# Performance work log

Measured on AMD Instinct MI355X. Metric: run time of the kernel, lower is better.

The kernel has to match this reference:

```python
import jax, jax.numpy as jnp
import numpy as np

F_DIM = 64; HID = 64; HEADS = 2; DH = 32; NG = 4; EPS = 1e-5; SCALE = 8.0  # sqrt(hid_dim)
B = 4; H = 64; W = 64; S = 8; CIN = 64


def _ln(x, g, b):
    mu = x.mean(-1, keepdims=True)
    var = ((x - mu) ** 2).mean(-1, keepdims=True)
    return (x - mu) * jax.lax.rsqrt(var + EPS) * g + b


def _gn(x, g, b):
    # x: [b, C, H, W]; normalize per group over (C/NG, H, W)
    bb, c, hh, ww = x.shape
    xg = x.reshape(bb, NG, -1)
    mu = xg.mean(-1, keepdims=True)
    var = ((xg - mu) ** 2).mean(-1, keepdims=True)
    xn = ((xg - mu) * jax.lax.rsqrt(var + EPS)).reshape(bb, c, hh, ww)
    return xn * g[None, :, None, None] + b[None, :, None, None]


def _mha(xq, xkv, qw, qb, kw, kb, vw, vb, ow, ob):
    # per-head attention with scaling by sqrt(hid_dim) (as in the source)
    q = xq @ qw + qb
    k = xkv @ kw + kb
    v = xkv @ vw + vb
    bb, l, _ = q.shape
    m = k.shape[1]
    qh = q.reshape(bb, l, HEADS, DH)
    kh = k.reshape(bb, m, HEADS, DH)
    vh = v.reshape(bb, m, HEADS, DH)
    s = jnp.einsum('blhd,bmhd->bhlm', qh, kh) / SCALE
    p = jax.nn.softmax(s, axis=-1)
    z = jnp.einsum('bhlm,bmhd->blhd', p, vh).reshape(bb, l, HID)
    return z @ ow + ob


def setup_inputs() -> dict:
    key = jax.random.key(0)
    ks = jax.random.split(key, 34)
    p = lambda k, shp: (jax.random.normal(k, shp, jnp.float32) * 0.02)
    d = {
        'x': jax.random.normal(ks[0], (B, H, W, F_DIM), jnp.float32),
        'slots': jax.random.normal(ks[1], (B, S, CIN), jnp.float32),
        'conv1_w': p(ks[2], (F_DIM, F_DIM)), 'conv1_b': p(ks[3], (F_DIM,)),
        'conv2_w': p(ks[4], (F_DIM, F_DIM)), 'conv2_b': p(ks[5], (F_DIM,)),
        'gn_g': jnp.ones((F_DIM,), jnp.float32), 'gn_b': jnp.zeros((F_DIM,), jnp.float32),
        'ln2_g': jnp.ones((F_DIM,), jnp.float32), 'ln2_b': jnp.zeros((F_DIM,), jnp.float32),
        'ln3_g': jnp.ones((F_DIM,), jnp.float32), 'ln3_b': jnp.zeros((F_DIM,), jnp.float32),
        'ln4_g': jnp.ones((F_DIM,), jnp.float32), 'ln4_b': jnp.zeros((F_DIM,), jnp.float32),
        'sa_qw': p(ks[6], (F_DIM, HID)), 'sa_qb': p(ks[7], (HID,)),
        'sa_kw': p(ks[8], (F_DIM, HID)), 'sa_kb': p(ks[9], (HID,)),
        'sa_vw': p(ks[10], (F_DIM, HID)), 'sa_vb': p(ks[11], (HID,)),
        'sa_ow': p(ks[12], (HID, F_DIM)), 'sa_ob': p(ks[13], (F_DIM,)),
        'ca_qw': p(ks[14], (F_DIM, HID)), 'ca_qb': p(ks[15], (HID,)),
        'ca_kw': p(ks[16], (CIN, HID)), 'ca_kb': p(ks[17], (HID,)),
        'ca_vw': p(ks[18], (CIN, HID)), 'ca_vb': p(ks[19], (HID,)),
        'ca_ow': p(ks[20], (HID, F_DIM)), 'ca_ob': p(ks[21], (F_DIM,)),
        'ff1_w': p(ks[22], (F_DIM, F_DIM)), 'ff1_b': p(ks[23], (F_DIM,)),
    }
    return d


def reference(x, slots, conv1_w, conv1_b, conv2_w, conv2_b, gn_g, gn_b,
              ln2_g, ln2_b, ln3_g, ln3_b, ln4_g, ln4_b,
              sa_qw, sa_qb, sa_kw, sa_kb, sa_vw, sa_vb, sa_ow, sa_ob,
              ca_qw, ca_qb, ca_kw, ca_kb, ca_vw, ca_vb, ca_ow, ca_ob,
              ff1_w, ff1_b):
    b, h, w, f = x.shape
    xc = jnp.transpose(x, (0, 3, 1, 2))               # [b,f,h,w]
    xc = _gn(xc, gn_g, gn_b)
    xc = jnp.einsum('bchw,oc->bohw', xc, conv1_w) + conv1_b[None, :, None, None]
    # faithful to torch: .contiguous().view(b,-1,f) on channels-first layout
    xs = xc.reshape(b, h * w, f)
    # repeat = 1
    xs = jax.nn.gelu(_ln(_mha(xs, xs, sa_qw, sa_qb, sa_kw, sa_kb, sa_vw, sa_vb, sa_ow, sa_ob), ln2_g, ln2_b) + xs, approximate=False)
    xs = _ln(_mha(xs, slots, ca_qw, ca_qb, ca_kw, ca_kb, ca_vw, ca_vb, ca_ow, ca_ob), ln3_g, ln3_b) + xs
    xs = _ln(xs @ ff1_w + ff1_b, ln4_g, ln4_b) + xs
    xo = jnp.transpose(xs.reshape(b, h, w, f), (0, 3, 1, 2))
    xo = jnp.einsum('bchw,oc->bohw', xo, conv2_w) + conv2_b[None, :, None, None]
    return jnp.transpose(xo, (0, 2, 3, 1))
```

## Files before the change

### kernel.cpp

```cpp
#include <hip/hip_runtime.h>
#include <hip/hip_bf16.h>
#include <math.h>

#define NBATCH 4
#define LTOK   4096
#define FD     64
#define NIT    16

typedef __attribute__((ext_vector_type(8))) short short8v;
typedef __attribute__((ext_vector_type(4))) float f32x4;

static __device__ inline uint32_t packbf2(float a, float b) {
    float2 f; f.x = a; f.y = b;
    __hip_bfloat162 h = __float22bfloat162_rn(f);
    uint32_t u; __builtin_memcpy(&u, &h, 4);
    return u;
}
static __device__ inline ushort packbf1(float a) {
    __hip_bfloat16 h = __float2bfloat16(a);
    ushort u; __builtin_memcpy(&u, &h, 2);
    return u;
}
static __device__ inline float gelu_exact(float y) {
    return 0.5f * y * (1.0f + erff(y * 0.70710678118654752f));
}

__global__ void gn_part_kernel(const float* __restrict__ x,
                               float* __restrict__ partS, float* __restrict__ partSS) {
    const int b = blockIdx.x >> 6, c = blockIdx.x & 63;
    const int t = threadIdx.x, l = t & 63, wv = t >> 6;
    const float4* xb = (const float4*)(x + (size_t)b * 262144) + (size_t)c * 1024;
    float s = 0.f, ss = 0.f;
#pragma unroll
    for (int k = 0; k < 4; k++) {
        float4 v = xb[t + 256 * k];
        s += (v.x + v.y) + (v.z + v.w);
        ss += (v.x * v.x + v.y * v.y) + (v.z * v.z + v.w * v.w);
    }
#pragma unroll
    for (int o = 0; o < 4; o++) {
        const int off = (int[]){1, 2, 16, 32}[o];
        s += __shfl_xor(s, off, 64);
        ss += __shfl_xor(ss, off, 64);
    }
    __shared__ float ls_s[4][4], ls_ss[4][4];
    if ((l & 51) == 0) { ls_s[wv][(l >> 2) & 3] = s; ls_ss[wv][(l >> 2) & 3] = ss; }
    __syncthreads();
    if (t < 4) {
        float S = 0.f, SS = 0.f;
#pragma unroll
        for (int w2 = 0; w2 < 4; w2++) { S += ls_s[w2][t]; SS += ls_ss[w2][t]; }
        partS[b * 256 + t * 64 + c] = S;
        partSS[b * 256 + t * 64 + c] = SS;
    }
}

__global__ void gn_conv1_kernel(const float* __restrict__ x,
                                const float* __restrict__ partS, const float* __restrict__ partSS,
                                const float* __restrict__ gg, const float* __restrict__ gb,
                                const float* __restrict__ w, const float* __restrict__ bias,
                                float* __restrict__ out) {
    const int b = blockIdx.x >> 6, i = blockIdx.x & 63;
    const int t = threadIdx.x;
    __shared__ float xn[64][65];
    __shared__ float wsm[64][64];
    __shared__ float sm[4], sr[4];
    {
        float sv = partS[b * 256 + t];
        float ssv = partSS[b * 256 + t];
        for (int o = 32; o; o >>= 1) { sv += __shfl_xor(sv, o, 64); ssv += __shfl_xor(ssv, o, 64); }
        if ((t & 63) == 0) {
            float mean = sv * (1.f / 65536.f);
            float var = ssv * (1.f / 65536.f) - mean * mean;
            sm[t >> 6] = mean;
            sr[t >> 6] = rsqrtf(var + 1e-5f);
        }
    }
    __syncthreads();
    {
        const int j = t >> 2, c0 = (t & 3) * 16, g = c0 >> 4;
        const float mean = sm[g], rstd = sr[g];
        const float* src = x + (((size_t)b * 64 + i) * 64 + j) * 64 + c0;
#pragma unroll
        for (int k = 0; k < 4; k++) {
            float4 v = *(const float4*)(src + 4 * k);
            xn[j][c0 + 4 * k + 0] = (v.x - mean) * rstd * gg[c0 + 4 * k + 0] + gb[c0 + 4 * k + 0];
            xn[j][c0 + 4 * k + 1] = (v.y - mean) * rstd * gg[c0 + 4 * k + 1] + gb[c0 + 4 * k + 1];
            xn[j][c0 + 4 * k + 2] = (v.z - mean) * rstd * gg[c0 + 4 * k + 2] + gb[c0 + 4 * k + 2];
            xn[j][c0 + 4 * k + 3] = (v.w - mean) * rstd * gg[c0 + 4 * k + 3] + gb[c0 + 4 * k + 3];
        }
        const int o = t >> 2, cc0 = (t & 3) * 16;
#pragma unroll
        for (int k = 0; k < 16; k++) wsm[cc0 + k][o] = w[o * 64 + cc0 + k];
    }
    __syncthreads();
    const int jj = t & 63, olo = (t >> 6) * 16;
    float acc[16];
#pragma unroll
    for (int oi = 0; oi < 16; oi++) acc[oi] = bias[olo + oi];
    for (int c = 0; c < 64; c++) {
        float xv = xn[jj][c];
#pragma unroll
        for (int oi = 0; oi < 16; oi++) acc[oi] += xv * wsm[c][olo + oi];
    }
#pragma unroll
    for (int oi = 0; oi < 16; oi++)
        out[((size_t)b * LTOK + (size_t)(olo + oi) * 64 + i) * 64 + jj] = acc[oi];
}

__global__ void qkv_kernel(const float* __restrict__ in,
                           const float* __restrict__ qw, const float* __restrict__ qb,
                           const float* __restrict__ kw, const float* __restrict__ kb,
                           const float* __restrict__ vw, const float* __restrict__ vb,
                           ushort* __restrict__ Qo, ushort* __restrict__ Ko, ushort* __restrict__ VTg) {
    __shared__ float xt[64][68];
    __shared__ float wt[64][64];
    __shared__ ushort vtr[64 * 72];
    const int t = threadIdx.x;
    const int ph = blockIdx.y;
    const size_t tok0 = (size_t)blockIdx.x * 64;
    const int b = blockIdx.x >> 6;
    const int tokb0 = (blockIdx.x & 63) * 64;
    const int r = t >> 2, cq = t & 3, olo = cq * 16;
    const float* W = (ph == 0) ? qw : (ph == 1) ? kw : vw;
    const float* Bb = (ph == 0) ? qb : (ph == 1) ? kb : vb;
    {
        const float4* src = (const float4*)(in + tok0 * 64) + (size_t)t * 4;
        float4* dst = (float4*)&xt[r][olo];
#pragma unroll
        for (int k = 0; k < 4; k++) dst[k] = src[k];
        const float4* ws2 = (const float4*)W + (size_t)t * 4;
        float4* wd = (float4*)wt + (size_t)t * 4;
#pragma unroll
        for (int k = 0; k < 4; k++) wd[k] = ws2[k];
    }
    __syncthreads();
    float acc[16];
#pragma unroll
    for (int k = 0; k < 4; k++) {
        float4 bv = *(const float4*)(Bb + olo + 4 * k);
        acc[4 * k] = bv.x; acc[4 * k + 1] = bv.y; acc[4 * k + 2] = bv.z; acc[4 * k + 3] = bv.w;
    }
    for (int f = 0; f < 64; f++) {
        float xv = xt[r][f];
#pragma unroll
        for (int oi = 0; oi < 16; oi++) acc[oi] += xv * wt[f][olo + oi];
    }
    if (ph < 2) {
        const float sc = (ph == 0) ? 0.180336880111f : 1.0f;
        uint32_t u[8];
#pragma unroll
        for (int i = 0; i < 8; i++) u[i] = packbf2(acc[2 * i] * sc, acc[2 * i + 1] * sc);
        ushort* op = (ph == 0 ? Qo : Ko) + (tok0 + r) * 64 + olo;
        *(uint4*)op = make_uint4(u[0], u[1], u[2], u[3]);
        *(uint4*)(op + 8) = make_uint4(u[4], u[5], u[6], u[7]);
    } else {
#pragma unroll
        for (int oi = 0; oi < 16; oi++) vtr[(olo + oi) * 72 + r] = packbf1(acc[oi]);
        __syncthreads();
        const int o = t >> 2, ch = t & 3;
        uint4 a0 = *(const uint4*)&vtr[o * 72 + ch * 16];
        uint4 a1 = *(const uint4*)&vtr[o * 72 + ch * 16 + 8];
        ushort* op = VTg + (size_t)(b * 64 + o) * 4096 + tokb0 + ch * 16;
        *(uint4*)op = a0;
        *(uint4*)(op + 8) = a1;
    }
}

__global__ __launch_bounds__(256) void flash_mfma(const ushort* __restrict__ Q,
                                                  const ushort* __restrict__ K,
                                                  const ushort* __restrict__ VTg,
                                                  float* __restrict__ Zp0, float* __restrict__ Zp1,
                                                  float* __restrict__ Zp2, float* __restrict__ Zp3,
                                                  float* __restrict__ Ls) {
    const int qt = blockIdx.x;
    const int bh = blockIdx.y;
    const int ks = blockIdx.z;
    const int b = bh >> 1, h = bh & 1;
    const int t = threadIdx.x;
    const int w = t >> 6, l = t & 63, lg = l >> 4, lq = l & 15;

    __shared__ ushort KsB[2][2048];
    __shared__ ushort VTB[2][2048];
    __shared__ ushort Pl[4096];

    const size_t base = (size_t)b * LTOK * 64 + h * 32;
    const size_t vrow0 = (size_t)(b * 64 + h * 32);

    const short8v qf = *(const short8v*)(Q + base + (size_t)(qt * 64 + w * 16 + lq) * 64 + 8 * lg);

    const int krow = t >> 2, kdg = t & 3;
    const int koff = ((krow << 5) + kdg * 8) ^ ((krow & 7) << 3);
    const int vrow = t >> 3, vc8 = t & 7;
    const int voff = ((vrow << 6) + vc8 * 8) ^ ((vrow & 7) << 3);
    const ushort* kgp = K + base + (size_t)(ks * NIT * 64 + krow) * 64 + kdg * 8;
    const ushort* vgp = VTg + (vrow0 + vrow) * 4096 + ks * NIT * 64 + vc8 * 8;

    *(uint4*)&KsB[0][koff] = *(const uint4*)kgp;  kgp += 64 * 64;
    *(uint4*)&VTB[0][voff] = *(const uint4*)vgp;  vgp += 64;

    f32x4 accZ[2];
#pragma unroll
    for (int d = 0; d < 2; d++) accZ[d] = (f32x4){0.f, 0.f, 0.f, 0.f};
    float lacc = 0.0f;
    const f32x4 zero4 = {0.f, 0.f, 0.f, 0.f};
    const int pb = w << 10;

    auto body = [&](const ushort* Kc, const ushort* Vc, ushort* Kn, ushort* Vn, bool pref) {
        __syncthreads();
        uint4 kq = make_uint4(0, 0, 0, 0), vq = make_uint4(0, 0, 0, 0);
        if (pref) {
            kq = *(const uint4*)kgp; kgp += 64 * 64;
            vq = *(const uint4*)vgp; vgp += 64;
        }
        f32x4 s4[4];
#pragma unroll
        for (int tk = 0; tk < 4; tk++) {
            const int kr = tk * 16 + lq;
            const short8v aK = *(const short8v*)&Kc[((kr << 5) + lg * 8) ^ ((lq & 7) << 3)];
            s4[tk] = __builtin_amdgcn_mfma_f32_16x16x32_bf16(aK, qf, zero4, 0, 0, 0);
        }
        uint32_t pw[8];
#pragma unroll
        for (int tk = 0; tk < 4; tk++) {
            float p0 = __builtin_amdgcn_exp2f(s4[tk][0]);
            float p1 = __builtin_amdgcn_exp2f(s4[tk][1]);
            float p2 = __builtin_amdgcn_exp2f(s4[tk][2]);
            float p3 = __builtin_amdgcn_exp2f(s4[tk][3]);
            lacc += (p0 + p1) + (p2 + p3);
            pw[2 * tk]     = packbf2(p0, p1);
            pw[2 * tk + 1] = packbf2(p2, p3);
        }
#pragma unroll
        for (int tk = 0; tk < 4; tk++) {
            const int idx = ((lq << 6) + tk * 16 + lg * 4) ^ ((lq & 7) << 3);
            *(uint2*)&Pl[pb + idx] = make_uint2(pw[2 * tk], pw[2 * tk + 1]);
        }
#pragma unroll
        for (int kc = 0; kc < 2; kc++) {
            const int ia = ((lq << 6) + kc * 32 + lg * 8) ^ ((lq & 7) << 3);
            const short8v aP = *(const short8v*)&Pl[pb + ia];
#pragma unroll
            for (int dt = 0; dt < 2; dt++) {
                const int ib = (((dt * 16 + lq) << 6) + kc * 32 + lg * 8) ^ ((lq & 7) << 3);
                const short8v bV = *(const short8v*)&Vc[ib];
                accZ[dt] = __builtin_amdgcn_mfma_f32_16x16x32_bf16(aP, bV, accZ[dt], 0, 0, 0);
            }
        }
        if (pref) {
            *(uint4*)&Kn[koff] = kq;
            *(uint4*)&Vn[voff] = vq;
        }
    };

#pragma unroll 1
    for (int it = 0; it < NIT / 2; it++) {
        body(KsB[0], VTB[0], KsB[1], VTB[1], true);
        body(KsB[1], VTB[1], KsB[0], VTB[0], it < NIT / 2 - 1);
    }

    float* Zo = (ks == 0) ? Zp0 : (ks == 1) ? Zp1 : (ks == 2) ? Zp2 : Zp3;
#pragma unroll
    for (int rr = 0; rr < 4; rr++) {
        const int qrow = qt * 64 + w * 16 + lg * 4 + rr;
#pragma unroll
        for (int dt = 0; dt < 2; dt++)
            Zo[base + (size_t)qrow * 64 + dt * 16 + lq] = accZ[dt][rr];
    }
    lacc += __shfl_xor(lacc, 16, 64);
    lacc += __shfl_xor(lacc, 32, 64);
    if (l < 16)
        Ls[ks * 32768 + bh * 4096 + qt * 64 + w * 16 + lq] = lacc;
}

__global__ __launch_bounds__(512) void tail_fused(
    const float* __restrict__ Zp0, const float* __restrict__ Zp1,
    const float* __restrict__ Zp2, const float* __restrict__ Zp3,
    const float* __restrict__ Ls, const float* __restrict__ xs0,
    const float* __restrict__ slots,
    const float* __restrict__ ckw, const float* __restrict__ ckb,
    const float* __restrict__ cvw, const float* __restrict__ cvb,
    const float* __restrict__ ow, const float* __restrict__ ob,
    const float* __restrict__ g2, const float* __restrict__ b2,
    const float* __restrict__ qw, const float* __restrict__ qb,
    const float* __restrict__ cow, const float* __restrict__ cob,
    const float* __restrict__ g3, const float* __restrict__ b3,
    const float* __restrict__ fw, const float* __restrict__ fb,
    const float* __restrict__ g4, const float* __restrict__ b4,
    const float* __restrict__ cw, const float* __restrict__ cb,
    float* __restrict__ out)
{
    const int t = threadIdx.x;
    const size_t tok0 = (size_t)blockIdx.x * 64;
    const int b = blockIdx.x >> 6;
    const int r = t >> 3, c = t & 7, olo = c * 8;
    __shared__ float xt[64][68];
    __shared__ float wt[64][64];
    __shared__ float kcs[512], vcs[512], sls[512];

    float acc[8], res[8];

    auto stage_w = [&](const float* W) {
        ((float4*)wt)[2 * t] = ((const float4*)W)[2 * t];
        ((float4*)wt)[2 * t + 1] = ((const float4*)W)[2 * t + 1];
    };
    auto stage_x_res = [&]() {
        float4* xd = (float4*)&xt[r][olo];
        xd[0] = make_float4(res[0], res[1], res[2], res[3]);
        xd[1] = make_float4(res[4], res[5], res[6], res[7]);
    };
    auto load8 = [&](float* dst, const float* p) {
        float4 u0 = *(const float4*)(p + olo);
        float4 u1 = *(const float4*)(p + olo + 4);
        dst[0] = u0.x; dst[1] = u0.y; dst[2] = u0.z; dst[3] = u0.w;
        dst[4] = u1.x; dst[5] = u1.y; dst[6] = u1.z; dst[7] = u1.w;
    };
    auto mm = [&](const float* bias) {
        load8(acc, bias);
        for (int f = 0; f < 64; f++) {
            float xv = xt[r][f];
#pragma unroll
            for (int oi = 0; oi < 8; oi++) acc[oi] += xv * wt[f][olo + oi];
        }
    };
    auto ln = [&](const float* gv, const float* bv, bool dogelu) {
        float s1 = 0.f, s2 = 0.f;
#pragma unroll
        for (int oi = 0; oi < 8; oi++) { s1 += acc[oi]; s2 += acc[oi] * acc[oi]; }
#pragma unroll
        for (int o = 1; o <= 4; o <<= 1) {
            s1 += __shfl_xor(s1, o, 64);
            s2 += __shfl_xor(s2, o, 64);
        }
        float mean = s1 * (1.f / 64.f);
        float var = s2 * (1.f / 64.f) - mean * mean;
        float rstd = rsqrtf(var + 1e-5f);
        float gl[8], bl[8];
        load8(gl, gv); load8(bl, bv);
#pragma unroll
        for (int oi = 0; oi < 8; oi++) {
            float y = (acc[oi] - mean) * rstd * gl[oi] + bl[oi] + res[oi];
            res[oi] = dogelu ? gelu_exact(y) : y;
        }
    };

    {
        if (t < 128) ((float4*)sls)[t] = ((const float4*)(slots + (size_t)b * 512))[t];
        const float4* z0 = (const float4*)(Zp0 + tok0 * 64);
        const float4* z1 = (const float4*)(Zp1 + tok0 * 64);
        const float4* z2 = (const float4*)(Zp2 + tok0 * 64);
        const float4* z3 = (const float4*)(Zp3 + tok0 * 64);
        float4 a0 = z0[2 * t], a1 = z0[2 * t + 1];
        float4 b0 = z1[2 * t], b1 = z1[2 * t + 1];
        float4 c0 = z2[2 * t], c1 = z2[2 * t + 1];
        float4 d0 = z3[2 * t], d1 = z3[2 * t + 1];
        const int hh = olo >> 5;
        const int bh_ = b * 2 + hh;
        const int tokb = (blockIdx.x & 63) * 64 + r;
        const float lt = Ls[bh_ * 4096 + tokb] + Ls[32768 + bh_ * 4096 + tokb]
                       + Ls[65536 + bh_ * 4096 + tokb] + Ls[98304 + bh_ * 4096 + tokb];
        const float inv = 1.0f / lt;
        float4* xd = (float4*)&xt[r][olo];
        xd[0] = make_float4(((a0.x + b0.x) + (c0.x + d0.x)) * inv,
                            ((a0.y + b0.y) + (c0.y + d0.y)) * inv,
                            ((a0.z + b0.z) + (c0.z + d0.z)) * inv,
                            ((a0.w + b0.w) + (c0.w + d0.w)) * inv);
        xd[1] = make_float4(((a1.x + b1.x) + (c1.x + d1.x)) * inv,
                            ((a1.y + b1.y) + (c1.y + d1.y)) * inv,
                            ((a1.z + b1.z) + (c1.z + d1.z)) * inv,
                            ((a1.w + b1.w) + (c1.w + d1.w)) * inv);
        stage_w(ow);
        float4 r0 = *(const float4*)(xs0 + (tok0 + r) * 64 + olo);
        float4 r1 = *(const float4*)(xs0 + (tok0 + r) * 64 + olo + 4);
        res[0] = r0.x; res[1] = r0.y; res[2] = r0.z; res[3] = r0.w;
        res[4] = r1.x; res[5] = r1.y; res[6] = r1.z; res[7] = r1.w;
    }
    __syncthreads();
    {
        const int j = t >> 6, o = t & 63;
        float ak = ckb[o], av = cvb[o];
#pragma unroll 8
        for (int c2 = 0; c2 < 64; c2++) {
            float sv = sls[j * 64 + c2];
            ak += sv * ckw[c2 * 64 + o];
            av += sv * cvw[c2 * 64 + o];
        }
        kcs[t] = ak; vcs[t] = av;
    }
    mm(ob);
    ln(g2, b2, true);

    __syncthreads();
    stage_x_res();
    stage_w(qw);
    __syncthreads();
    mm(qb);
    {
        float p[8];
        float mx = -3.0e38f;
#pragma unroll
        for (int j = 0; j < 8; j++) {
            float d = 0.f;
#pragma unroll
            for (int i2 = 0; i2 < 8; i2++) d += acc[i2] * kcs[j * 64 + olo + i2];
            d += __shfl_xor(d, 1, 64);
            d += __shfl_xor(d, 2, 64);
            d *= 0.125f;
            p[j] = d;
            mx = fmaxf(mx, d);
        }
        float es = 0.f;
#pragma unroll
        for (int j = 0; j < 8; j++) { p[j] = __expf(p[j] - mx); es += p[j]; }
        float inv = 1.f / es;
#pragma unroll
        for (int oi = 0; oi < 8; oi++) {
            float z = 0.f;
#pragma unroll
            for (int j = 0; j < 8; j++) z += p[j] * vcs[j * 64 + olo + oi];
            acc[oi] = z * inv;
        }
    }

    __syncthreads();
    {
        float4* xd = (float4*)&xt[r][olo];
        xd[0] = make_float4(acc[0], acc[1], acc[2], acc[3]);
        xd[1] = make_float4(acc[4], acc[5], acc[6], acc[7]);
    }
    stage_w(cow);
    __syncthreads();
    mm(cob);
    ln(g3, b3, false);

    __syncthreads();
    stage_x_res();
    stage_w(fw);
    __syncthreads();
    mm(fb);
    ln(g4, b4, false);

    __syncthreads();
    stage_x_res();
    {
        const int o5 = t >> 3, c5 = (t & 7) * 8;
#pragma unroll
        for (int k = 0; k < 8; k++) wt[c5 + k][o5] = cw[o5 * 64 + c5 + k];
    }
    __syncthreads();
    mm(cb);
    float* op = out + (tok0 + r) * 64 + olo;
    *(float4*)op = make_float4(acc[0], acc[1], acc[2], acc[3]);
    *(float4*)(op + 4) = make_float4(acc[4], acc[5], acc[6], acc[7]);
}

extern "C" void kernel_launch(void* const* d_in, const int* in_sizes, int n_in,
                              void* d_out, int out_size, void* d_ws, size_t ws_size,
                              hipStream_t stream) {
    const float* x       = (const float*)d_in[0];
    const float* slots   = (const float*)d_in[1];
    const float* conv1_w = (const float*)d_in[2];
    const float* conv1_b = (const float*)d_in[3];
    const float* conv2_w = (const float*)d_in[4];
    const float* conv2_b = (const float*)d_in[5];
    const float* gn_g    = (const float*)d_in[6];
    const float* gn_b    = (const float*)d_in[7];
    const float* ln2_g   = (const float*)d_in[8];
    const float* ln2_b   = (const float*)d_in[9];
    const float* ln3_g   = (const float*)d_in[10];
    const float* ln3_b   = (const float*)d_in[11];
    const float* ln4_g   = (const float*)d_in[12];
    const float* ln4_b   = (const float*)d_in[13];
    const float* sa_qw   = (const float*)d_in[14];
    const float* sa_qb   = (const float*)d_in[15];
    const float* sa_kw   = (const float*)d_in[16];
    const float* sa_kb   = (const float*)d_in[17];
    const float* sa_vw   = (const float*)d_in[18];
    const float* sa_vb   = (const float*)d_in[19];
    const float* sa_ow   = (const float*)d_in[20];
    const float* sa_ob   = (const float*)d_in[21];
    const float* ca_qw   = (const float*)d_in[22];
    const float* ca_qb   = (const float*)d_in[23];
    const float* ca_kw   = (const float*)d_in[24];
    const float* ca_kb   = (const float*)d_in[25];
    const float* ca_vw   = (const float*)d_in[26];
    const float* ca_vb   = (const float*)d_in[27];
    const float* ca_ow   = (const float*)d_in[28];
    const float* ca_ob   = (const float*)d_in[29];
    const float* ff1_w   = (const float*)d_in[30];
    const float* ff1_b   = (const float*)d_in[31];

    float* ws = (float*)d_ws;
    const size_t NBUF = (size_t)NBATCH * LTOK * FD;
    float* partS  = ws;
    float* partSS = ws + 1024;
    float* A      = ws + 4096;
    ushort* Kb    = (ushort*)(A + NBUF);
    ushort* VTgb  = Kb + NBUF;
    ushort* Qb    = VTgb + NBUF;
    float* Zp1    = (float*)(Qb + NBUF);
    float* Zp2    = Zp1 + NBUF;
    float* Zp3    = Zp2 + NBUF;
    float* Ls     = Zp3 + NBUF;
    float* Zp0    = (float*)d_out;

    gn_part_kernel<<<256, 256, 0, stream>>>(x, partS, partSS);
    gn_conv1_kernel<<<256, 256, 0, stream>>>(x, partS, partSS, gn_g, gn_b, conv1_w, conv1_b, A);
    qkv_kernel<<<dim3(256, 3), 256, 0, stream>>>(A, sa_qw, sa_qb, sa_kw, sa_kb, sa_vw, sa_vb, Qb, Kb, VTgb);
    flash_mfma<<<dim3(64, 8, 4), 256, 0, stream>>>(Qb, Kb, VTgb, Zp0, Zp1, Zp2, Zp3, Ls);
    tail_fused<<<256, 512, 0, stream>>>(Zp0, Zp1, Zp2, Zp3, Ls, A, slots,
                                        ca_kw, ca_kb, ca_vw, ca_vb,
                                        sa_ow, sa_ob, ln2_g, ln2_b,
                                        ca_qw, ca_qb, ca_ow, ca_ob, ln3_g, ln3_b,
                                        ff1_w, ff1_b, ln4_g, ln4_b,
                                        conv2_w, conv2_b, (float*)d_out);
}
```

Measured before the change: 95.21 us.

## Use 32x32x16 MFMA in flash attention with register-shuffled P, split tail blocks

The flash attention kernel moves from 16x16x32 MFMA tiles to 32x32x16 tiles, giving each wave 32 query rows, so each block covers 128 queries. The probability matrix is rearranged between half-waves with cross-lane shuffles instead of going through shared memory. This removes the LDS round trip for P and halves the number of K/V tile loads per query, at the cost of extra shuffles and more accumulator registers. The tail kernel is also resized to 32 tokens per block with 256 threads, doubling its block count.

```diff
diff --git a/kernel.cpp b/kernel.cpp
--- a/kernel.cpp
+++ b/kernel.cpp
@@ -5,10 +5,12 @@
 #define NBATCH 4
 #define LTOK   4096
 #define FD     64
+#define KSPLIT 4
 #define NIT    16
 
 typedef __attribute__((ext_vector_type(8))) short short8v;
 typedef __attribute__((ext_vector_type(4))) float f32x4;
+typedef __attribute__((ext_vector_type(16))) float f32x16;
 
 static __device__ inline uint32_t packbf2(float a, float b) {
     float2 f; f.x = a; f.y = b;
@@ -178,16 +180,17 @@
     const int ks = blockIdx.z;
     const int b = bh >> 1, h = bh & 1;
     const int t = threadIdx.x;
-    const int w = t >> 6, l = t & 63, lg = l >> 4, lq = l & 15;
+    const int w = t >> 6, l = t & 63, lq = l & 31, sig = l >> 5;
 
     __shared__ ushort KsB[2][2048];
     __shared__ ushort VTB[2][2048];
-    __shared__ ushort Pl[4096];
 
     const size_t base = (size_t)b * LTOK * 64 + h * 32;
     const size_t vrow0 = (size_t)(b * 64 + h * 32);
 
-    const short8v qf = *(const short8v*)(Q + base + (size_t)(qt * 64 + w * 16 + lq) * 64 + 8 * lg);
+    const int qrow = qt * 128 + w * 32 + lq;
+    const short8v qf0 = *(const short8v*)(Q + base + (size_t)qrow * 64 + 8 * sig);
+    const short8v qf1 = *(const short8v*)(Q + base + (size_t)qrow * 64 + 16 + 8 * sig);
 
     const int krow = t >> 2, kdg = t & 3;
     const int koff = ((krow << 5) + kdg * 8) ^ ((krow & 7) << 3);
@@ -199,12 +202,13 @@
     *(uint4*)&KsB[0][koff] = *(const uint4*)kgp;  kgp += 64 * 64;
     *(uint4*)&VTB[0][voff] = *(const uint4*)vgp;  vgp += 64;
 
-    f32x4 accZ[2];
-#pragma unroll
-    for (int d = 0; d < 2; d++) accZ[d] = (f32x4){0.f, 0.f, 0.f, 0.f};
+    f32x16 accZ;
+#pragma unroll
+    for (int i = 0; i < 16; i++) accZ[i] = 0.f;
+    f32x16 zero16;
+#pragma unroll
+    for (int i = 0; i < 16; i++) zero16[i] = 0.f;
     float lacc = 0.0f;
-    const f32x4 zero4 = {0.f, 0.f, 0.f, 0.f};
-    const int pb = w << 10;
 
     auto body = [&](const ushort* Kc, const ushort* Vc, ushort* Kn, ushort* Vn, bool pref) {
         __syncthreads();
@@ -213,39 +217,37 @@
             kq = *(const uint4*)kgp; kgp += 64 * 64;
             vq = *(const uint4*)vgp; vgp += 64;
         }
-        f32x4 s4[4];
-#pragma unroll
-        for (int tk = 0; tk < 4; tk++) {
-            const int kr = tk * 16 + lq;
-            const short8v aK = *(const short8v*)&Kc[((kr << 5) + lg * 8) ^ ((lq & 7) << 3)];
-            s4[tk] = __builtin_amdgcn_mfma_f32_16x16x32_bf16(aK, qf, zero4, 0, 0, 0);
-        }
-        uint32_t pw[8];
-#pragma unroll
-        for (int tk = 0; tk < 4; tk++) {
-            float p0 = __builtin_amdgcn_exp2f(s4[tk][0]);
-            float p1 = __builtin_amdgcn_exp2f(s4[tk][1]);
-            float p2 = __builtin_amdgcn_exp2f(s4[tk][2]);
-            float p3 = __builtin_amdgcn_exp2f(s4[tk][3]);
-            lacc += (p0 + p1) + (p2 + p3);
-            pw[2 * tk]     = packbf2(p0, p1);
-            pw[2 * tk + 1] = packbf2(p2, p3);
-        }
-#pragma unroll
-        for (int tk = 0; tk < 4; tk++) {
-            const int idx = ((lq << 6) + tk * 16 + lg * 4) ^ ((lq & 7) << 3);
-            *(uint2*)&Pl[pb + idx] = make_uint2(pw[2 * tk], pw[2 * tk + 1]);
-        }
-#pragma unroll
-        for (int kc = 0; kc < 2; kc++) {
-            const int ia = ((lq << 6) + kc * 32 + lg * 8) ^ ((lq & 7) << 3);
-            const short8v aP = *(const short8v*)&Pl[pb + ia];
-#pragma unroll
-            for (int dt = 0; dt < 2; dt++) {
-                const int ib = (((dt * 16 + lq) << 6) + kc * 32 + lg * 8) ^ ((lq & 7) << 3);
-                const short8v bV = *(const short8v*)&Vc[ib];
-                accZ[dt] = __builtin_amdgcn_mfma_f32_16x16x32_bf16(aP, bV, accZ[dt], 0, 0, 0);
+#pragma unroll
+        for (int kb2 = 0; kb2 < 2; kb2++) {
+            const int kb = kb2 * 32;
+            const int kr = kb + lq;
+            const short8v aK0 = *(const short8v*)&Kc[((kr << 5) + 8 * sig) ^ ((kr & 7) << 3)];
+            const short8v aK1 = *(const short8v*)&Kc[((kr << 5) + 16 + 8 * sig) ^ ((kr & 7) << 3)];
+            f32x16 st = __builtin_amdgcn_mfma_f32_32x32x16_bf16(aK0, qf0, zero16, 0, 0, 0);
+            st = __builtin_amdgcn_mfma_f32_32x32x16_bf16(aK1, qf1, st, 0, 0, 0);
+            uint32_t pk[8];
+#pragma unroll
+            for (int i = 0; i < 8; i++) {
+                float p0 = __builtin_amdgcn_exp2f(st[2 * i]);
+                float p1 = __builtin_amdgcn_exp2f(st[2 * i + 1]);
+                lacc += p0 + p1;
+                pk[i] = packbf2(p0, p1);
             }
+            const uint32_t r1 = __shfl_xor(sig ? pk[0] : pk[2], 32, 64);
+            const uint32_t r2 = __shfl_xor(sig ? pk[1] : pk[3], 32, 64);
+            const uint32_t r3 = __shfl_xor(sig ? pk[4] : pk[6], 32, 64);
+            const uint32_t r4 = __shfl_xor(sig ? pk[5] : pk[7], 32, 64);
+            uint4 A0 = make_uint4(sig ? r1 : pk[0], sig ? r2 : pk[1],
+                                  sig ? pk[2] : r1, sig ? pk[3] : r2);
+            uint4 A1 = make_uint4(sig ? r3 : pk[4], sig ? r4 : pk[5],
+                                  sig ? pk[6] : r3, sig ? pk[7] : r4);
+            short8v aP0, aP1;
+            __builtin_memcpy(&aP0, &A0, 16);
+            __builtin_memcpy(&aP1, &A1, 16);
+            const short8v vt0 = *(const short8v*)&Vc[((lq << 6) + kb + 8 * sig) ^ ((lq & 7) << 3)];
+            const short8v vt1 = *(const short8v*)&Vc[((lq << 6) + kb + 16 + 8 * sig) ^ ((lq & 7) << 3)];
+            accZ = __builtin_amdgcn_mfma_f32_32x32x16_bf16(aP0, vt0, accZ, 0, 0, 0);
+            accZ = __builtin_amdgcn_mfma_f32_32x32x16_bf16(aP1, vt1, accZ, 0, 0, 0);
         }
         if (pref) {
             *(uint4*)&Kn[koff] = kq;
@@ -261,19 +263,16 @@
 
     float* Zo = (ks == 0) ? Zp0 : (ks == 1) ? Zp1 : (ks == 2) ? Zp2 : Zp3;
 #pragma unroll
-    for (int rr = 0; rr < 4; rr++) {
-        const int qrow = qt * 64 + w * 16 + lg * 4 + rr;
-#pragma unroll
-        for (int dt = 0; dt < 2; dt++)
-            Zo[base + (size_t)qrow * 64 + dt * 16 + lq] = accZ[dt][rr];
-    }
-    lacc += __shfl_xor(lacc, 16, 64);
+    for (int r = 0; r < 16; r++) {
+        const int qr = qt * 128 + w * 32 + (r & 3) + 8 * (r >> 2) + 4 * sig;
+        Zo[base + (size_t)qr * 64 + lq] = accZ[r];
+    }
     lacc += __shfl_xor(lacc, 32, 64);
-    if (l < 16)
-        Ls[ks * 32768 + bh * 4096 + qt * 64 + w * 16 + lq] = lacc;
-}
-
-__global__ __launch_bounds__(512) void tail_fused(
+    if (l < 32)
+        Ls[ks * 32768 + bh * 4096 + qt * 128 + w * 32 + lq] = lacc;
+}
+
+__global__ __launch_bounds__(256) void tail_fused(
     const float* __restrict__ Zp0, const float* __restrict__ Zp1,
     const float* __restrict__ Zp2, const float* __restrict__ Zp3,
     const float* __restrict__ Ls, const float* __restrict__ xs0,
@@ -291,18 +290,19 @@
     float* __restrict__ out)
 {
     const int t = threadIdx.x;
-    const size_t tok0 = (size_t)blockIdx.x * 64;
-    const int b = blockIdx.x >> 6;
+    const size_t tok0 = (size_t)blockIdx.x * 32;
+    const int b = blockIdx.x >> 7;
     const int r = t >> 3, c = t & 7, olo = c * 8;
-    __shared__ float xt[64][68];
+    __shared__ float xt[32][68];
     __shared__ float wt[64][64];
     __shared__ float kcs[512], vcs[512], sls[512];
 
     float acc[8], res[8];
 
     auto stage_w = [&](const float* W) {
-        ((float4*)wt)[2 * t] = ((const float4*)W)[2 * t];
-        ((float4*)wt)[2 * t + 1] = ((const float4*)W)[2 * t + 1];
+#pragma unroll
+        for (int k = 0; k < 4; k++)
+            ((float4*)wt)[4 * t + k] = ((const float4*)W)[4 * t + k];
     };
     auto stage_x_res = [&]() {
         float4* xd = (float4*)&xt[r][olo];
@@ -356,7 +356,7 @@
         float4 d0 = z3[2 * t], d1 = z3[2 * t + 1];
         const int hh = olo >> 5;
         const int bh_ = b * 2 + hh;
-        const int tokb = (blockIdx.x & 63) * 64 + r;
+        const int tokb = (blockIdx.x & 127) * 32 + r;
         const float lt = Ls[bh_ * 4096 + tokb] + Ls[32768 + bh_ * 4096 + tokb]
                        + Ls[65536 + bh_ * 4096 + tokb] + Ls[98304 + bh_ * 4096 + tokb];
         const float inv = 1.0f / lt;
@@ -376,8 +376,8 @@
         res[4] = r1.x; res[5] = r1.y; res[6] = r1.z; res[7] = r1.w;
     }
     __syncthreads();
-    {
-        const int j = t >> 6, o = t & 63;
+    for (int jo = t; jo < 512; jo += 256) {
+        const int j = jo >> 6, o = jo & 63;
         float ak = ckb[o], av = cvb[o];
 #pragma unroll 8
         for (int c2 = 0; c2 < 64; c2++) {
@@ -385,7 +385,7 @@
             ak += sv * ckw[c2 * 64 + o];
             av += sv * cvw[c2 * 64 + o];
         }
-        kcs[t] = ak; vcs[t] = av;
+        kcs[jo] = ak; vcs[jo] = av;
     }
     mm(ob);
     ln(g2, b2, true);
@@ -443,9 +443,9 @@
     __syncthreads();
     stage_x_res();
     {
-        const int o5 = t >> 3, c5 = (t & 7) * 8;
-#pragma unroll
-        for (int k = 0; k < 8; k++) wt[c5 + k][o5] = cw[o5 * 64 + c5 + k];
+        const int o5 = t >> 2, c5 = (t & 3) * 16;
+#pragma unroll
+        for (int k = 0; k < 16; k++) wt[c5 + k][o5] = cw[o5 * 64 + c5 + k];
     }
     __syncthreads();
     mm(cb);
@@ -507,8 +507,8 @@
     gn_part_kernel<<<256, 256, 0, stream>>>(x, partS, partSS);
     gn_conv1_kernel<<<256, 256, 0, stream>>>(x, partS, partSS, gn_g, gn_b, conv1_w, conv1_b, A);
     qkv_kernel<<<dim3(256, 3), 256, 0, stream>>>(A, sa_qw, sa_qb, sa_kw, sa_kb, sa_vw, sa_vb, Qb, Kb, VTgb);
-    flash_mfma<<<dim3(64, 8, 4), 256, 0, stream>>>(Qb, Kb, VTgb, Zp0, Zp1, Zp2, Zp3, Ls);
-    tail_fused<<<256, 512, 0, stream>>>(Zp0, Zp1, Zp2, Zp3, Ls, A, slots,
+    flash_mfma<<<dim3(32, 8, KSPLIT), 256, 0, stream>>>(Qb, Kb, VTgb, Zp0, Zp1, Zp2, Zp3, Ls);
+    tail_fused<<<512, 256, 0, stream>>>(Zp0, Zp1, Zp2, Zp3, Ls, A, slots,
                                         ca_kw, ca_kb, ca_vw, ca_vb,
                                         sa_ow, sa_ob, ln2_g, ln2_b,
                                         ca_qw, ca_qb, ca_ow, ca_ob, ln3_g, ln3_b,
```

New measurement: 94.54 us. No clear change (-0.7%).
